# Optimization experiments

Measured on AMD Instinct MI355X. Metric: run time of the kernel, lower is better.

Reference implementation:

```python
import jax, jax.numpy as jnp
import numpy as np

B, N, DIM, H, DH = 4, 2048, 768, 12, 64

def layer_norm_no_affine(x, eps=1e-5):
    mu = jnp.mean(x, axis=-1, keepdims=True)
    var = jnp.var(x, axis=-1, keepdims=True)
    return (x - mu) / jnp.sqrt(var + eps)

def setup_inputs() -> dict:
    key = jax.random.key(0)
    ks = jax.random.split(key, 6)
    s = 1.0 / np.sqrt(DIM)
    return {
        "x": jax.random.normal(ks[0], (B, N, DIM), dtype=jnp.float32),
        "gamma": jnp.zeros((DIM,), dtype=jnp.float32),
        "Wq": jax.random.normal(ks[1], (DIM, DIM), dtype=jnp.float32) * s,
        "Wk": jax.random.normal(ks[2], (DIM, DIM), dtype=jnp.float32) * s,
        "Wv": jax.random.normal(ks[3], (DIM, DIM), dtype=jnp.float32) * s,
        "Wo": jax.random.normal(ks[4], (DIM, DIM), dtype=jnp.float32) * s,
    }

def reference(x, gamma, Wq, Wk, Wv, Wo):
    scale = DH ** -0.5
    xn = layer_norm_no_affine(x) * (gamma + 1.0)  # [b,n,dim]
    # projections (torch Linear: y = x @ W.T), split heads b n (h d) -> b h n d
    def proj(t, W):
        return (t @ W.T).reshape(B, N, H, DH).transpose(0, 2, 1, 3)
    q = proj(xn, Wq) * scale
    k = proj(xn, Wk)
    v = proj(xn, Wv)
    qk_sim = jnp.einsum('bhid,bhjd->bhij', q, k)  # full N x N scores (unfused)
    attn = jax.nn.softmax(qk_sim, axis=-1)
    out = jnp.einsum('bhij,bhjd->bhid', attn, v)
    out = out.transpose(0, 2, 1, 3).reshape(B, N, H * DH)
    return out @ Wo.T
```

## Files before the change

### kernel.cpp

```cpp
#include <hip/hip_runtime.h>
#include <stdint.h>

#define NSEQ 2048
#define NB 4
#define NH 12
#define MTOT 8192
#define DMODEL 768

typedef __attribute__((ext_vector_type(8))) short bfx8;
typedef __attribute__((ext_vector_type(4))) float fx4;
typedef __attribute__((ext_vector_type(16))) float fx16;

static __device__ __forceinline__ unsigned short f2bf(float f) {
  union { float f; unsigned u; } v; v.f = f;
  unsigned r = v.u + 0x7FFFu + ((v.u >> 16) & 1u);
  return (unsigned short)(r >> 16);
}

static __device__ __forceinline__ unsigned cvt_pk_bf16(float lo, float hi) {
  unsigned r;
  asm("v_cvt_pk_bf16_f32 %0, %1, %2" : "=v"(r) : "v"(lo), "v"(hi));
  return r;
}

static __device__ __forceinline__ void gload_lds16(const void* g, void* l) {
  __builtin_amdgcn_global_load_lds(
      (const __attribute__((address_space(1))) unsigned int*)g,
      (__attribute__((address_space(3))) unsigned int*)l, 16, 0, 0);
}

__global__ __launch_bounds__(256) void k_ln(const float* __restrict__ x,
                                            const float* __restrict__ gamma,
                                            unsigned short* __restrict__ xn) {
  int row = blockIdx.x * 4 + (threadIdx.x >> 6);
  int lane = threadIdx.x & 63;
  const float* xr = x + (size_t)row * DMODEL;
  float4 a = *(const float4*)(xr + lane * 4);
  float4 b = *(const float4*)(xr + 256 + lane * 4);
  float4 c = *(const float4*)(xr + 512 + lane * 4);
  float s  = a.x + a.y + a.z + a.w + b.x + b.y + b.z + b.w + c.x + c.y + c.z + c.w;
  float ss = a.x*a.x + a.y*a.y + a.z*a.z + a.w*a.w
           + b.x*b.x + b.y*b.y + b.z*b.z + b.w*b.w
           + c.x*c.x + c.y*c.y + c.z*c.z + c.w*c.w;
  #pragma unroll
  for (int off = 1; off < 64; off <<= 1) {
    s  += __shfl_xor(s, off);
    ss += __shfl_xor(ss, off);
  }
  float mu = s * (1.0f / 768.0f);
  float var = ss * (1.0f / 768.0f) - mu * mu;
  float rs = rsqrtf(var + 1e-5f);
  float4 ga = *(const float4*)(gamma + lane * 4);
  float4 gb = *(const float4*)(gamma + 256 + lane * 4);
  float4 gc = *(const float4*)(gamma + 512 + lane * 4);
  unsigned short* orow = xn + (size_t)row * DMODEL;
  ushort4 o;
  o.x = f2bf((a.x - mu) * rs * (ga.x + 1.0f));
  o.y = f2bf((a.y - mu) * rs * (ga.y + 1.0f));
  o.z = f2bf((a.z - mu) * rs * (ga.z + 1.0f));
  o.w = f2bf((a.w - mu) * rs * (ga.w + 1.0f));
  *(ushort4*)(orow + lane * 4) = o;
  o.x = f2bf((b.x - mu) * rs * (gb.x + 1.0f));
  o.y = f2bf((b.y - mu) * rs * (gb.y + 1.0f));
  o.z = f2bf((b.z - mu) * rs * (gb.z + 1.0f));
  o.w = f2bf((b.w - mu) * rs * (gb.w + 1.0f));
  *(ushort4*)(orow + 256 + lane * 4) = o;
  o.x = f2bf((c.x - mu) * rs * (gc.x + 1.0f));
  o.y = f2bf((c.y - mu) * rs * (gc.y + 1.0f));
  o.z = f2bf((c.z - mu) * rs * (gc.z + 1.0f));
  o.w = f2bf((c.w - mu) * rs * (gc.w + 1.0f));
  *(ushort4*)(orow + 512 + lane * 4) = o;
}

__global__ __launch_bounds__(256) void k_wconv(const float* __restrict__ w0,
                                               const float* __restrict__ w1,
                                               const float* __restrict__ w2,
                                               const float* __restrict__ w3,
                                               unsigned short* __restrict__ dst) {
  int which = blockIdx.y;
  const float* src = (which == 0) ? w0 : (which == 1) ? w1 : (which == 2) ? w2 : w3;
  size_t idx = ((size_t)blockIdx.x * 256 + threadIdx.x) * 4;
  float4 v = *(const float4*)(src + idx);
  ushort4 o;
  o.x = f2bf(v.x); o.y = f2bf(v.y); o.z = f2bf(v.z); o.w = f2bf(v.w);
  *(ushort4*)(dst + (size_t)which * (DMODEL * DMODEL) + idx) = o;
}

template<int MODE>
__global__ __launch_bounds__(256) void k_gemm(const unsigned short* __restrict__ A,
                                              const unsigned short* __restrict__ Bbase,
                                              unsigned short* __restrict__ q_o,
                                              unsigned short* __restrict__ k_o,
                                              unsigned short* __restrict__ v_o,
                                              float* __restrict__ f_o) {
  __shared__ unsigned short At[2][128 * 32];
  __shared__ unsigned short Bt[2][128 * 32];
  int t = threadIdx.x;
  int w = t >> 6, lane = t & 63;
  int wr = w >> 1, wc = w & 1;
  int g = lane >> 4, cc = lane & 15;
  int mbase = blockIdx.x * 128;
  int by = blockIdx.y;
  const unsigned short* Bp;
  int ncolbase;
  if (MODE == 0) {
    int which = by / 6;
    Bp = Bbase + (size_t)which * (DMODEL * DMODEL);
    ncolbase = (by % 6) * 128;
  } else {
    Bp = Bbase;
    ncolbase = by * 128;
  }
  int srow = lane >> 2;
  int schunk = (lane & 3) * 8;
  const unsigned short* Asrc = A  + (size_t)(mbase   + w * 32 + srow) * DMODEL + schunk;
  const unsigned short* Bsrc = Bp + (size_t)(ncolbase + w * 32 + srow) * DMODEL + schunk;

  auto stage = [&](int ks, int buf) {
    gload_lds16(Asrc + ks,               &At[buf][(w * 32) * 32]);
    gload_lds16(Asrc + ks + 16 * DMODEL, &At[buf][(w * 32 + 16) * 32]);
    gload_lds16(Bsrc + ks,               &Bt[buf][(w * 32) * 32]);
    gload_lds16(Bsrc + ks + 16 * DMODEL, &Bt[buf][(w * 32 + 16) * 32]);
  };

  fx4 acc[4][4];
  #pragma unroll
  for (int i = 0; i < 4; ++i)
    #pragma unroll
    for (int j = 0; j < 4; ++j)
      acc[i][j] = (fx4){0.f, 0.f, 0.f, 0.f};

  stage(0, 0);
  for (int ks = 0; ks < DMODEL; ks += 32) {
    int buf = (ks >> 5) & 1;
    __syncthreads();
    if (ks + 32 < DMODEL) stage(ks + 32, buf ^ 1);
    bfx8 af[4], bfr[4];
    #pragma unroll
    for (int mi = 0; mi < 4; ++mi)
      af[mi] = *(const bfx8*)(&At[buf][(wr * 64 + mi * 16 + cc) * 32 + g * 8]);
    #pragma unroll
    for (int ni = 0; ni < 4; ++ni)
      bfr[ni] = *(const bfx8*)(&Bt[buf][(wc * 64 + ni * 16 + cc) * 32 + g * 8]);
    #pragma unroll
    for (int mi = 0; mi < 4; ++mi)
      #pragma unroll
      for (int ni = 0; ni < 4; ++ni)
        acc[mi][ni] = __builtin_amdgcn_mfma_f32_16x16x32_bf16(af[mi], bfr[ni], acc[mi][ni], 0, 0, 0);
  }

  if (MODE == 0) {
    int which = by / 6;
    if (which < 2) {
      unsigned short* dst = (which == 0) ? q_o : k_o;
      float fs = (which == 0) ? 0.18033688f : 1.0f;
      #pragma unroll
      for (int mi = 0; mi < 4; ++mi) {
        #pragma unroll
        for (int ni = 0; ni < 4; ++ni) {
          int n = (by % 6) * 128 + wc * 64 + ni * 16 + cc;
          int h = n >> 6, dd = n & 63;
          #pragma unroll
          for (int r = 0; r < 4; ++r) {
            int m = mbase + wr * 64 + mi * 16 + g * 4 + r;
            int bb = m >> 11, nq = m & 2047;
            dst[((size_t)(bb * NH + h) * NSEQ + nq) * 64 + dd] = f2bf(acc[mi][ni][r] * fs);
          }
        }
      }
    } else {
      #pragma unroll
      for (int mi = 0; mi < 4; ++mi) {
        #pragma unroll
        for (int ni = 0; ni < 4; ++ni) {
          int n = (by % 6) * 128 + wc * 64 + ni * 16 + cc;
          int h = n >> 6, dd = n & 63;
          int m0 = mbase + wr * 64 + mi * 16 + g * 4;
          int bb = m0 >> 11, nq = m0 & 2047;
          ushort4 pk;
          pk.x = f2bf(acc[mi][ni][0]);
          pk.y = f2bf(acc[mi][ni][1]);
          pk.z = f2bf(acc[mi][ni][2]);
          pk.w = f2bf(acc[mi][ni][3]);
          *(ushort4*)(v_o + ((size_t)(bb * NH + h) * 64 + dd) * NSEQ + nq) = pk;
        }
      }
    }
  } else {
    #pragma unroll
    for (int mi = 0; mi < 4; ++mi)
      #pragma unroll
      for (int ni = 0; ni < 4; ++ni) {
        int n = by * 128 + wc * 64 + ni * 16 + cc;
        #pragma unroll
        for (int r = 0; r < 4; ++r) {
          int m = mbase + wr * 64 + mi * 16 + g * 4 + r;
          f_o[(size_t)m * DMODEL + n] = acc[mi][ni][r];
        }
      }
  }
}

__global__ __launch_bounds__(256, 3) void k_attn(const unsigned short* __restrict__ qw,
                                                 const unsigned short* __restrict__ kw,
                                                 const unsigned short* __restrict__ vtw,
                                                 unsigned short* __restrict__ ao) {
  __shared__ unsigned short Kb[2][64 * 64];
  __shared__ unsigned short Vb[3][64 * 64];
  int bid = blockIdx.x;
  int xcd = bid & 7, jj = bid >> 3;
  int bh = xcd * 6 + (jj >> 4);
  int qt = jj & 15;
  int t = threadIdx.x;
  int w = t >> 6, lane = t & 63;
  int c = lane & 31, b5 = lane >> 5;
  int q0 = qt * 128 + w * 32;
  const unsigned short* qp = qw + (size_t)bh * NSEQ * 64;
  const unsigned char* kby = (const unsigned char*)(kw  + (size_t)bh * NSEQ * 64);
  const unsigned char* vby = (const unsigned char*)(vtw + (size_t)bh * 64 * NSEQ);

  int srow = lane >> 3;
  int scol = (((lane & 7) ^ srow) << 4);
  int ch0 = 2 * w, ch1 = 2 * w + 1;

  auto stageK = [&](int tt, int buf) {
    gload_lds16(kby + (size_t)(tt * 64 + ch0 * 8 + srow) * 128 + scol, &Kb[buf][ch0 * 512]);
    gload_lds16(kby + (size_t)(tt * 64 + ch1 * 8 + srow) * 128 + scol, &Kb[buf][ch1 * 512]);
  };
  auto stageV = [&](int tt, int buf) {
    gload_lds16(vby + (size_t)(ch0 * 8 + srow) * 4096 + tt * 128 + scol, &Vb[buf][ch0 * 512]);
    gload_lds16(vby + (size_t)(ch1 * 8 + srow) * 4096 + tt * 128 + scol, &Vb[buf][ch1 * 512]);
  };

  bfx8 qf[4];
  #pragma unroll
  for (int dc = 0; dc < 4; ++dc)
    qf[dc] = *(const bfx8*)(qp + (size_t)(q0 + c) * 64 + dc * 16 + b5 * 8);

  fx16 o0, o1;
  #pragma unroll
  for (int i = 0; i < 16; ++i) { o0[i] = 0.f; o1[i] = 0.f; }
  float l_run = 0.f;
  int rsw = (c & 7) << 4;

  fx16 sA0, sA1, sB0, sB1;

  auto qk = [&](int tt, fx16& d0, fx16& d1) {
    const unsigned char* Kbb = (const unsigned char*)&Kb[tt & 1][0];
    #pragma unroll
    for (int i = 0; i < 16; ++i) { d0[i] = 0.f; d1[i] = 0.f; }
    __builtin_amdgcn_s_setprio(1);
    #pragma unroll
    for (int dc = 0; dc < 4; ++dc) {
      bfx8 kf0 = *(const bfx8*)(Kbb + (c) * 128      + ((dc * 32 + b5 * 16) ^ rsw));
      bfx8 kf1 = *(const bfx8*)(Kbb + (32 + c) * 128 + ((dc * 32 + b5 * 16) ^ rsw));
      d0 = __builtin_amdgcn_mfma_f32_32x32x16_bf16(kf0, qf[dc], d0, 0, 0, 0);
      d1 = __builtin_amdgcn_mfma_f32_32x32x16_bf16(kf1, qf[dc], d1, 0, 0, 0);
    }
    __builtin_amdgcn_s_setprio(0);
  };

  auto softmax_pv = [&](int pv_t, fx16& p0, fx16& p1) {
    #pragma unroll
    for (int i = 0; i < 16; ++i) {
      p0[i] = __builtin_amdgcn_exp2f(p0[i]);
      p1[i] = __builtin_amdgcn_exp2f(p1[i]);
    }
    float ps = 0.f;
    #pragma unroll
    for (int i = 0; i < 16; ++i) ps += p0[i] + p1[i];
    ps += __shfl_xor(ps, 32);
    l_run += ps;
    bfx8 pf[4];
    #pragma unroll
    for (int half = 0; half < 2; ++half) {
      {
        unsigned w0 = cvt_pk_bf16(p0[8 * half + 0], p0[8 * half + 1]);
        unsigned w1 = cvt_pk_bf16(p0[8 * half + 2], p0[8 * half + 3]);
        unsigned w2 = cvt_pk_bf16(p0[8 * half + 4], p0[8 * half + 5]);
        unsigned w3 = cvt_pk_bf16(p0[8 * half + 6], p0[8 * half + 7]);
        asm("v_permlane32_swap_b32 %0, %1" : "+v"(w0), "+v"(w2));
        asm("v_permlane32_swap_b32 %0, %1" : "+v"(w1), "+v"(w3));
        uint4 u = make_uint4(w0, w1, w2, w3);
        pf[half] = *(bfx8*)&u;
      }
      {
        unsigned w0 = cvt_pk_bf16(p1[8 * half + 0], p1[8 * half + 1]);
        unsigned w1 = cvt_pk_bf16(p1[8 * half + 2], p1[8 * half + 3]);
        unsigned w2 = cvt_pk_bf16(p1[8 * half + 4], p1[8 * half + 5]);
        unsigned w3 = cvt_pk_bf16(p1[8 * half + 6], p1[8 * half + 7]);
        asm("v_permlane32_swap_b32 %0, %1" : "+v"(w0), "+v"(w2));
        asm("v_permlane32_swap_b32 %0, %1" : "+v"(w1), "+v"(w3));
        uint4 u = make_uint4(w0, w1, w2, w3);
        pf[2 + half] = *(bfx8*)&u;
      }
    }
    const unsigned char* Vbb = (const unsigned char*)&Vb[pv_t % 3][0];
    __builtin_amdgcn_s_setprio(1);
    #pragma unroll
    for (int kc = 0; kc < 4; ++kc) {
      bfx8 vf0 = *(const bfx8*)(Vbb + (c) * 128      + ((kc * 32 + b5 * 16) ^ rsw));
      bfx8 vf1 = *(const bfx8*)(Vbb + (32 + c) * 128 + ((kc * 32 + b5 * 16) ^ rsw));
      o0 = __builtin_amdgcn_mfma_f32_32x32x16_bf16(vf0, pf[kc], o0, 0, 0, 0);
      o1 = __builtin_amdgcn_mfma_f32_32x32x16_bf16(vf1, pf[kc], o1, 0, 0, 0);
    }
    __builtin_amdgcn_s_setprio(0);
  };

  auto body = [&](int tt, fx16& cur0, fx16& cur1, fx16& prv0, fx16& prv1) {
    __syncthreads();
    qk(tt, cur0, cur1);
    if (tt + 1 < 32) { stageK(tt + 1, (tt + 1) & 1); stageV(tt + 1, (tt + 1) % 3); }
    softmax_pv(tt - 1, prv0, prv1);
  };

  stageK(0, 0); stageV(0, 0);
  __syncthreads();
  qk(0, sA0, sA1);
  stageK(1, 1); stageV(1, 1);

  for (int tp = 1; tp < 31; tp += 2) {
    body(tp,     sB0, sB1, sA0, sA1);
    body(tp + 1, sA0, sA1, sB0, sB1);
  }
  body(31, sB0, sB1, sA0, sA1);
  softmax_pv(31, sB0, sB1);

  float inv = 1.0f / l_run;
  int b = bh / NH, h = bh % NH;
  unsigned short* orow = ao + (size_t)(b * NSEQ + q0 + c) * DMODEL + h * 64;
  #pragma unroll
  for (int k = 0; k < 4; ++k) {
    ushort4 pk;
    pk.x = f2bf(o0[4 * k + 0] * inv);
    pk.y = f2bf(o0[4 * k + 1] * inv);
    pk.z = f2bf(o0[4 * k + 2] * inv);
    pk.w = f2bf(o0[4 * k + 3] * inv);
    *(ushort4*)(orow + 8 * k + 4 * b5) = pk;
    pk.x = f2bf(o1[4 * k + 0] * inv);
    pk.y = f2bf(o1[4 * k + 1] * inv);
    pk.z = f2bf(o1[4 * k + 2] * inv);
    pk.w = f2bf(o1[4 * k + 3] * inv);
    *(ushort4*)(orow + 32 + 8 * k + 4 * b5) = pk;
  }
}

extern "C" void kernel_launch(void* const* d_in, const int* in_sizes, int n_in,
                              void* d_out, int out_size, void* d_ws, size_t ws_size,
                              hipStream_t stream) {
  const float* x     = (const float*)d_in[0];
  const float* gamma = (const float*)d_in[1];
  const float* Wq    = (const float*)d_in[2];
  const float* Wk    = (const float*)d_in[3];
  const float* Wv    = (const float*)d_in[4];
  const float* Wo    = (const float*)d_in[5];
  float* out = (float*)d_out;

  unsigned short* xn  = (unsigned short*)d_ws;
  unsigned short* wbf = xn  + (size_t)MTOT * DMODEL;
  unsigned short* qws = wbf + (size_t)4 * DMODEL * DMODEL;
  unsigned short* kws = qws + (size_t)MTOT * DMODEL;
  unsigned short* vtws = kws + (size_t)MTOT * DMODEL;
  unsigned short* aow = vtws + (size_t)MTOT * DMODEL;

  k_ln<<<MTOT / 4, 256, 0, stream>>>(x, gamma, xn);
  k_wconv<<<dim3(576, 4), 256, 0, stream>>>(Wq, Wk, Wv, Wo, wbf);
  k_gemm<0><<<dim3(64, 18), 256, 0, stream>>>(xn, wbf, qws, kws, vtws, nullptr);
  k_attn<<<768, 256, 0, stream>>>(qws, kws, vtws, aow);
  k_gemm<1><<<dim3(64, 6), 256, 0, stream>>>(aow, wbf + (size_t)3 * DMODEL * DMODEL,
                                             nullptr, nullptr, nullptr, out);
}
```

Baseline: 141.5 us.

## Merge LayerNorm and weight-convert kernels; use power-of-two V ring buffer

Merges the layer-norm and weight bf16 conversion kernels into one launch, with a block-index branch choosing which job each block does, which saves one kernel launch. In the attention kernel, K and V staging move into a single 48KB byte array. The V ring grows from 3 to 4 buffers so the slot index is a mask rather than a mod-3. The swizzled LDS fragment offsets are also precomputed once into registers. The larger LDS footprint (48KB vs 40KB) could reduce attention occupancy below the 3 blocks per CU the launch bounds target.

```diff
diff --git a/kernel.cpp b/kernel.cpp
--- a/kernel.cpp
+++ b/kernel.cpp
@@ -29,61 +29,64 @@
       (__attribute__((address_space(3))) unsigned int*)l, 16, 0, 0);
 }
 
-__global__ __launch_bounds__(256) void k_ln(const float* __restrict__ x,
-                                            const float* __restrict__ gamma,
-                                            unsigned short* __restrict__ xn) {
-  int row = blockIdx.x * 4 + (threadIdx.x >> 6);
-  int lane = threadIdx.x & 63;
-  const float* xr = x + (size_t)row * DMODEL;
-  float4 a = *(const float4*)(xr + lane * 4);
-  float4 b = *(const float4*)(xr + 256 + lane * 4);
-  float4 c = *(const float4*)(xr + 512 + lane * 4);
-  float s  = a.x + a.y + a.z + a.w + b.x + b.y + b.z + b.w + c.x + c.y + c.z + c.w;
-  float ss = a.x*a.x + a.y*a.y + a.z*a.z + a.w*a.w
-           + b.x*b.x + b.y*b.y + b.z*b.z + b.w*b.w
-           + c.x*c.x + c.y*c.y + c.z*c.z + c.w*c.w;
-  #pragma unroll
-  for (int off = 1; off < 64; off <<= 1) {
-    s  += __shfl_xor(s, off);
-    ss += __shfl_xor(ss, off);
-  }
-  float mu = s * (1.0f / 768.0f);
-  float var = ss * (1.0f / 768.0f) - mu * mu;
-  float rs = rsqrtf(var + 1e-5f);
-  float4 ga = *(const float4*)(gamma + lane * 4);
-  float4 gb = *(const float4*)(gamma + 256 + lane * 4);
-  float4 gc = *(const float4*)(gamma + 512 + lane * 4);
-  unsigned short* orow = xn + (size_t)row * DMODEL;
-  ushort4 o;
-  o.x = f2bf((a.x - mu) * rs * (ga.x + 1.0f));
-  o.y = f2bf((a.y - mu) * rs * (ga.y + 1.0f));
-  o.z = f2bf((a.z - mu) * rs * (ga.z + 1.0f));
-  o.w = f2bf((a.w - mu) * rs * (ga.w + 1.0f));
-  *(ushort4*)(orow + lane * 4) = o;
-  o.x = f2bf((b.x - mu) * rs * (gb.x + 1.0f));
-  o.y = f2bf((b.y - mu) * rs * (gb.y + 1.0f));
-  o.z = f2bf((b.z - mu) * rs * (gb.z + 1.0f));
-  o.w = f2bf((b.w - mu) * rs * (gb.w + 1.0f));
-  *(ushort4*)(orow + 256 + lane * 4) = o;
-  o.x = f2bf((c.x - mu) * rs * (gc.x + 1.0f));
-  o.y = f2bf((c.y - mu) * rs * (gc.y + 1.0f));
-  o.z = f2bf((c.z - mu) * rs * (gc.z + 1.0f));
-  o.w = f2bf((c.w - mu) * rs * (gc.w + 1.0f));
-  *(ushort4*)(orow + 512 + lane * 4) = o;
-}
-
-__global__ __launch_bounds__(256) void k_wconv(const float* __restrict__ w0,
-                                               const float* __restrict__ w1,
-                                               const float* __restrict__ w2,
-                                               const float* __restrict__ w3,
-                                               unsigned short* __restrict__ dst) {
-  int which = blockIdx.y;
-  const float* src = (which == 0) ? w0 : (which == 1) ? w1 : (which == 2) ? w2 : w3;
-  size_t idx = ((size_t)blockIdx.x * 256 + threadIdx.x) * 4;
-  float4 v = *(const float4*)(src + idx);
-  ushort4 o;
-  o.x = f2bf(v.x); o.y = f2bf(v.y); o.z = f2bf(v.z); o.w = f2bf(v.w);
-  *(ushort4*)(dst + (size_t)which * (DMODEL * DMODEL) + idx) = o;
+__global__ __launch_bounds__(256) void k_pre(const float* __restrict__ x,
+                                             const float* __restrict__ gamma,
+                                             const float* __restrict__ w0,
+                                             const float* __restrict__ w1,
+                                             const float* __restrict__ w2,
+                                             const float* __restrict__ w3,
+                                             unsigned short* __restrict__ xn,
+                                             unsigned short* __restrict__ wbf) {
+  int bx = blockIdx.x;
+  if (bx < 2048) {
+    int row = bx * 4 + (threadIdx.x >> 6);
+    int lane = threadIdx.x & 63;
+    const float* xr = x + (size_t)row * DMODEL;
+    float4 a = *(const float4*)(xr + lane * 4);
+    float4 b = *(const float4*)(xr + 256 + lane * 4);
+    float4 c = *(const float4*)(xr + 512 + lane * 4);
+    float s  = a.x + a.y + a.z + a.w + b.x + b.y + b.z + b.w + c.x + c.y + c.z + c.w;
+    float ss = a.x*a.x + a.y*a.y + a.z*a.z + a.w*a.w
+             + b.x*b.x + b.y*b.y + b.z*b.z + b.w*b.w
+             + c.x*c.x + c.y*c.y + c.z*c.z + c.w*c.w;
+    #pragma unroll
+    for (int off = 1; off < 64; off <<= 1) {
+      s  += __shfl_xor(s, off);
+      ss += __shfl_xor(ss, off);
+    }
+    float mu = s * (1.0f / 768.0f);
+    float var = ss * (1.0f / 768.0f) - mu * mu;
+    float rs = rsqrtf(var + 1e-5f);
+    float4 ga = *(const float4*)(gamma + lane * 4);
+    float4 gb = *(const float4*)(gamma + 256 + lane * 4);
+    float4 gc = *(const float4*)(gamma + 512 + lane * 4);
+    unsigned short* orow = xn + (size_t)row * DMODEL;
+    ushort4 o;
+    o.x = f2bf((a.x - mu) * rs * (ga.x + 1.0f));
+    o.y = f2bf((a.y - mu) * rs * (ga.y + 1.0f));
+    o.z = f2bf((a.z - mu) * rs * (ga.z + 1.0f));
+    o.w = f2bf((a.w - mu) * rs * (ga.w + 1.0f));
+    *(ushort4*)(orow + lane * 4) = o;
+    o.x = f2bf((b.x - mu) * rs * (gb.x + 1.0f));
+    o.y = f2bf((b.y - mu) * rs * (gb.y + 1.0f));
+    o.z = f2bf((b.z - mu) * rs * (gb.z + 1.0f));
+    o.w = f2bf((b.w - mu) * rs * (gb.w + 1.0f));
+    *(ushort4*)(orow + 256 + lane * 4) = o;
+    o.x = f2bf((c.x - mu) * rs * (gc.x + 1.0f));
+    o.y = f2bf((c.y - mu) * rs * (gc.y + 1.0f));
+    o.z = f2bf((c.z - mu) * rs * (gc.z + 1.0f));
+    o.w = f2bf((c.w - mu) * rs * (gc.w + 1.0f));
+    *(ushort4*)(orow + 512 + lane * 4) = o;
+  } else {
+    int b2 = bx - 2048;
+    int which = b2 / 576, bxx = b2 % 576;
+    const float* src = (which == 0) ? w0 : (which == 1) ? w1 : (which == 2) ? w2 : w3;
+    size_t idx = ((size_t)bxx * 256 + threadIdx.x) * 4;
+    float4 v = *(const float4*)(src + idx);
+    ushort4 o;
+    o.x = f2bf(v.x); o.y = f2bf(v.y); o.z = f2bf(v.z); o.w = f2bf(v.w);
+    *(ushort4*)(wbf + (size_t)which * (DMODEL * DMODEL) + idx) = o;
+  }
 }
 
 template<int MODE>
@@ -205,8 +208,7 @@
                                                  const unsigned short* __restrict__ kw,
                                                  const unsigned short* __restrict__ vtw,
                                                  unsigned short* __restrict__ ao) {
-  __shared__ unsigned short Kb[2][64 * 64];
-  __shared__ unsigned short Vb[3][64 * 64];
+  __shared__ __align__(16) unsigned char LBC[49152];
   int bid = blockIdx.x;
   int xcd = bid & 7, jj = bid >> 3;
   int bh = xcd * 6 + (jj >> 4);
@@ -223,13 +225,15 @@
   int scol = (((lane & 7) ^ srow) << 4);
   int ch0 = 2 * w, ch1 = 2 * w + 1;
 
-  auto stageK = [&](int tt, int buf) {
-    gload_lds16(kby + (size_t)(tt * 64 + ch0 * 8 + srow) * 128 + scol, &Kb[buf][ch0 * 512]);
-    gload_lds16(kby + (size_t)(tt * 64 + ch1 * 8 + srow) * 128 + scol, &Kb[buf][ch1 * 512]);
-  };
-  auto stageV = [&](int tt, int buf) {
-    gload_lds16(vby + (size_t)(ch0 * 8 + srow) * 4096 + tt * 128 + scol, &Vb[buf][ch0 * 512]);
-    gload_lds16(vby + (size_t)(ch1 * 8 + srow) * 4096 + tt * 128 + scol, &Vb[buf][ch1 * 512]);
+  auto stageK = [&](int tt) {
+    unsigned char* base = LBC + (tt & 1) * 8192;
+    gload_lds16(kby + (size_t)(tt * 64 + ch0 * 8 + srow) * 128 + scol, base + ch0 * 1024);
+    gload_lds16(kby + (size_t)(tt * 64 + ch1 * 8 + srow) * 128 + scol, base + ch1 * 1024);
+  };
+  auto stageV = [&](int tt) {
+    unsigned char* base = LBC + 16384 + (tt & 3) * 8192;
+    gload_lds16(vby + (size_t)(ch0 * 8 + srow) * 4096 + tt * 128 + scol, base + ch0 * 1024);
+    gload_lds16(vby + (size_t)(ch1 * 8 + srow) * 4096 + tt * 128 + scol, base + ch1 * 1024);
   };
 
   bfx8 qf[4];
@@ -237,23 +241,27 @@
   for (int dc = 0; dc < 4; ++dc)
     qf[dc] = *(const bfx8*)(qp + (size_t)(q0 + c) * 64 + dc * 16 + b5 * 8);
 
+  int la[4];
+  #pragma unroll
+  for (int dc = 0; dc < 4; ++dc)
+    la[dc] = c * 128 + ((dc * 32 + b5 * 16) ^ ((c & 7) << 4));
+
   fx16 o0, o1;
   #pragma unroll
   for (int i = 0; i < 16; ++i) { o0[i] = 0.f; o1[i] = 0.f; }
   float l_run = 0.f;
-  int rsw = (c & 7) << 4;
 
   fx16 sA0, sA1, sB0, sB1;
 
   auto qk = [&](int tt, fx16& d0, fx16& d1) {
-    const unsigned char* Kbb = (const unsigned char*)&Kb[tt & 1][0];
+    const unsigned char* Kbb = LBC + (tt & 1) * 8192;
     #pragma unroll
     for (int i = 0; i < 16; ++i) { d0[i] = 0.f; d1[i] = 0.f; }
     __builtin_amdgcn_s_setprio(1);
     #pragma unroll
     for (int dc = 0; dc < 4; ++dc) {
-      bfx8 kf0 = *(const bfx8*)(Kbb + (c) * 128      + ((dc * 32 + b5 * 16) ^ rsw));
-      bfx8 kf1 = *(const bfx8*)(Kbb + (32 + c) * 128 + ((dc * 32 + b5 * 16) ^ rsw));
+      bfx8 kf0 = *(const bfx8*)(Kbb + la[dc]);
+      bfx8 kf1 = *(const bfx8*)(Kbb + la[dc] + 4096);
       d0 = __builtin_amdgcn_mfma_f32_32x32x16_bf16(kf0, qf[dc], d0, 0, 0, 0);
       d1 = __builtin_amdgcn_mfma_f32_32x32x16_bf16(kf1, qf[dc], d1, 0, 0, 0);
     }
@@ -295,12 +303,12 @@
         pf[2 + half] = *(bfx8*)&u;
       }
     }
-    const unsigned char* Vbb = (const unsigned char*)&Vb[pv_t % 3][0];
+    const unsigned char* Vbb = LBC + 16384 + (pv_t & 3) * 8192;
     __builtin_amdgcn_s_setprio(1);
     #pragma unroll
     for (int kc = 0; kc < 4; ++kc) {
-      bfx8 vf0 = *(const bfx8*)(Vbb + (c) * 128      + ((kc * 32 + b5 * 16) ^ rsw));
-      bfx8 vf1 = *(const bfx8*)(Vbb + (32 + c) * 128 + ((kc * 32 + b5 * 16) ^ rsw));
+      bfx8 vf0 = *(const bfx8*)(Vbb + la[kc]);
+      bfx8 vf1 = *(const bfx8*)(Vbb + la[kc] + 4096);
       o0 = __builtin_amdgcn_mfma_f32_32x32x16_bf16(vf0, pf[kc], o0, 0, 0, 0);
       o1 = __builtin_amdgcn_mfma_f32_32x32x16_bf16(vf1, pf[kc], o1, 0, 0, 0);
     }
@@ -310,14 +318,14 @@
   auto body = [&](int tt, fx16& cur0, fx16& cur1, fx16& prv0, fx16& prv1) {
     __syncthreads();
     qk(tt, cur0, cur1);
-    if (tt + 1 < 32) { stageK(tt + 1, (tt + 1) & 1); stageV(tt + 1, (tt + 1) % 3); }
+    if (tt + 1 < 32) { stageK(tt + 1); stageV(tt + 1); }
     softmax_pv(tt - 1, prv0, prv1);
   };
 
-  stageK(0, 0); stageV(0, 0);
+  stageK(0); stageV(0);
   __syncthreads();
   qk(0, sA0, sA1);
-  stageK(1, 1); stageV(1, 1);
+  stageK(1); stageV(1);
 
   for (int tp = 1; tp < 31; tp += 2) {
     body(tp,     sB0, sB1, sA0, sA1);
@@ -363,8 +371,7 @@
   unsigned short* vtws = kws + (size_t)MTOT * DMODEL;
   unsigned short* aow = vtws + (size_t)MTOT * DMODEL;
 
-  k_ln<<<MTOT / 4, 256, 0, stream>>>(x, gamma, xn);
-  k_wconv<<<dim3(576, 4), 256, 0, stream>>>(Wq, Wk, Wv, Wo, wbf);
+  k_pre<<<4352, 256, 0, stream>>>(x, gamma, Wq, Wk, Wv, Wo, xn, wbf);
   k_gemm<0><<<dim3(64, 18), 256, 0, stream>>>(xn, wbf, qws, kws, vtws, nullptr);
   k_attn<<<768, 256, 0, stream>>>(qws, kws, vtws, aow);
   k_gemm<1><<<dim3(64, 6), 256, 0, stream>>>(aow, wbf + (size_t)3 * DMODEL * DMODEL,
```

Result: no change. 140.3 us (-0.9%).
